# Kernel optimization log

Measured on AMD Instinct MI355X. Metric: run time of the kernel, lower is better.

The kernel has to match this reference:

```python
import jax, jax.numpy as jnp
import numpy as np
from jax import lax

# ---- static config (from cfg) ----
B, NCLS, CREG, H, W = 16, 3, 50, 96, 320
K = 100                  # DETECTIONS_PER_IMG
DOWN = 4                 # BACKBONE.DOWN_RATIO
THRESH = 0.2             # DETECTIONS_THRESHOLD
IMG_W, IMG_H = W * DOWN, H * DOWN
EPS = 1e-6
# channel layout in pred_reg (kvper):
#  0:4 dim_2d | 4:6 offset_3d | 6:9 dim_3d | 9:25 orient | 25:45 corner_offset
#  45:48 corner_uncertainty | 48 depth | 49 depth_uncertainty


def setup_inputs() -> dict:
    key = jax.random.key(0)
    k1, k2, k3 = jax.random.split(key, 3)
    # shift heatmap logits negative so only a sparse set passes the threshold
    pred_hmp = jax.random.normal(k1, (B, NCLS, H, W), jnp.float32) * 2.0 - 2.0
    pred_reg = jax.random.normal(k2, (B, CREG, H, W), jnp.float32) * 0.5
    # KITTI P2 intrinsics: [f_u, c_u, f_v, c_v] per image
    calib = jnp.tile(jnp.array([[721.5377, 609.5593, 721.5377, 172.854]],
                               jnp.float32), (B, 1))
    pad_size = jnp.zeros((B, 2), jnp.float32)
    # per-class mean dims (l, h, w): Car / Pedestrian / Cyclist
    dim_mean = jnp.array([[3.88, 1.53, 1.63],
                          [0.84, 1.76, 0.66],
                          [1.76, 1.73, 0.60]], jnp.float32)
    return {"pred_hmp": pred_hmp, "pred_reg": pred_reg, "calib": calib,
            "pad_size": pad_size, "dim_mean": dim_mean}


def reference(pred_hmp, pred_reg, calib, pad_size, dim_mean):
    f32 = pred_hmp.dtype
    # ---- nms_hm: sigmoid + 3x3 max-pool suppression ----
    heat = jax.nn.sigmoid(pred_hmp)
    hmax = lax.reduce_window(heat, -jnp.inf, lax.max,
                             (1, 1, 3, 3), (1, 1, 1, 1), 'SAME')
    heat = jnp.where(hmax == heat, heat, jnp.zeros((), f32))
    # ---- select_topk (CenterNet-style): per-class topk then global topk ----
    flat = heat.reshape(B, NCLS, H * W)
    s1, i1 = lax.top_k(flat, K)                        # (B, C, K)
    s2, i2 = lax.top_k(s1.reshape(B, NCLS * K), K)     # (B, K)
    classes = i2 // K                                  # (B, K)
    inds = jnp.take_along_axis(i1.reshape(B, NCLS * K), i2, axis=1)  # flat h*w idx
    ys = (inds // W).astype(f32)
    xs = (inds % W).astype(f32)
    # ---- select_point_of_interest: gather 50-ch reg features at topk points ----
    regf = pred_reg.transpose(0, 2, 3, 1).reshape(B, H * W, CREG)
    pois = jnp.take_along_axis(regf, inds[:, :, None], axis=1).reshape(B * K, CREG)

    scores = s2.reshape(-1)                            # (N,) N = B*K
    cls = classes.reshape(-1)
    pts = jnp.stack([xs.reshape(-1), ys.reshape(-1)], axis=1)  # (N, 2)
    mask = (scores >= THRESH).astype(f32)
    bidx = jnp.repeat(jnp.arange(B), K)                # per-detection batch index

    reg2d = jax.nn.relu(pois[:, 0:4])                  # l, t, r, b
    off3d = pois[:, 4:6]
    dimoff = pois[:, 6:9]
    kpt = pois[:, 25:45].reshape(-1, 10, 2)            # 10 keypoints (x, y)
    cunc = jnp.exp(pois[:, 45:48])                     # corner uncertainty
    doff = pois[:, 48]
    dunc = jnp.exp(pois[:, 49:50])                     # direct depth uncertainty

    # ---- decode_dim3d: exp offset scaled by class mean dims ----
    dims = jnp.exp(dimoff) * dim_mean[cls]             # (N, 3); dims[:,1] = height
    h3d = dims[:, 1]

    # ---- decode_depth (inv_sigmoid) ----
    direct_depth = jnp.clip(1.0 / jax.nn.sigmoid(doff) - 1.0, 0.1, 100.0)

    # ---- decode_depth_from_kpts_batch: pinhole height -> depth ----
    fu = calib[bidx, 0]; cu = calib[bidx, 1]
    fv = calib[bidx, 2]; cv = calib[bidx, 3]
    ctr_h = kpt[:, 8, 1] - kpt[:, 9, 1]                       # bottom - top center
    c02_h = kpt[:, jnp.array([0, 2]), 1] - kpt[:, jnp.array([4, 6]), 1]
    c13_h = kpt[:, jnp.array([1, 3]), 1] - kpt[:, jnp.array([5, 7]), 1]
    d_ctr = fu * h3d / (jax.nn.relu(ctr_h) * DOWN + EPS)
    d_02 = ((fu * h3d)[:, None] / (jax.nn.relu(c02_h) * DOWN + EPS)).mean(axis=1)
    d_13 = ((fu * h3d)[:, None] / (jax.nn.relu(c13_h) * DOWN + EPS)).mean(axis=1)
    kpt_depths = jnp.clip(jnp.stack([d_ctr, d_02, d_13], axis=1), 0.1, 100.0)

    # ---- 'soft' depth ensemble: uncertainty-weighted average ----
    comb_d = jnp.concatenate([direct_depth[:, None], kpt_depths], axis=1)  # (N,4)
    comb_u = jnp.concatenate([dunc, cunc], axis=1)                          # (N,4)
    wts = 1.0 / comb_u
    wts = wts / wts.sum(axis=1, keepdims=True)
    depth = (comb_d * wts).sum(axis=1)
    depth_err = (wts * comb_u).sum(axis=1)

    # ---- decode_box2d_fcos ----
    pad = pad_size[bidx]                               # (N, 2)
    box2d = jnp.concatenate([pts - reg2d[:, :2], pts + reg2d[:, 2:]],
                            axis=1) * DOWN - jnp.tile(pad, (1, 2))
    hi = jnp.array([IMG_W - 1, IMG_H - 1, IMG_W - 1, IMG_H - 1], f32)
    box2d = jnp.clip(box2d, 0.0, hi)

    # ---- decode_loc3d: unproject projected 3D center at estimated depth ----
    proj = (pts + off3d) * DOWN - pad                  # (N, 2) image-plane uv
    x3 = (proj[:, 0] - cu) * depth / fu
    y3 = (proj[:, 1] - cv) * depth / fv
    loc3d = jnp.stack([x3, y3, depth], axis=1)

    result = jnp.concatenate([cls.astype(f32)[:, None], scores[:, None],
                              box2d, dims, loc3d, depth_err[:, None]], axis=1)
    return result * mask[:, None]                      # (B*K, 13)
```

## Files before the change

kernel.cpp:

```cpp
#include <hip/hip_runtime.h>
#include <math.h>


#define W_ 320
#define H_ 96
#define HW_ (W_ * H_)
#define CANDCAP 2048
#define SKEYCAP 512
#define BITS_02 0x3E4CCCCDu
#define FLAG_MAGIC 0x5EC0DE01

__device__ inline unsigned long long shflx64(unsigned long long v, int m) {
  int lo = __shfl_xor((int)(unsigned)v, m, 64);
  int hi = __shfl_xor((int)(unsigned)(v >> 32), m, 64);
  return ((unsigned long long)(unsigned)hi << 32) | (unsigned)lo;
}

__global__ __launch_bounds__(1024) void monoflex_all(
    const float* __restrict__ hmp,
    const float* __restrict__ reg,
    const float* __restrict__ calib,
    const float* __restrict__ pad_size,
    const float* __restrict__ dim_mean,
    float* __restrict__ out,
    unsigned long long* __restrict__ s1,
    int* __restrict__ flags) {
  const int ph = blockIdx.x;
  const int half = ph & 1;
  const int plane = ph >> 1;
  const int t = threadIdx.x;
  const int lane = t & 63;
  const float* p = hmp + (size_t)plane * HW_;
  const int r0 = half * 48;

  __shared__ unsigned long long cand[CANDCAP];
  __shared__ unsigned long long skey[SKEYCAP];
  __shared__ int hist[1024];
  __shared__ int cnt, mcnt, cutbin;
  __shared__ unsigned long long halfkeys[600];
  __shared__ unsigned long long classlist[300];
  __shared__ int selgi[100];
  __shared__ int selcls[100];
  __shared__ float selsc[100];
  __shared__ float pbuf[100 * 51];

  if (t == 0) { cnt = 0; mcnt = 0; cutbin = 0; }
  hist[t] = 0;
  __syncthreads();

  for (int idx = t; idx < 48 * W_; idx += 1024) {
    int rr = idx / W_;
    int c = idx - rr * W_;
    int r = r0 + rr;
    int g = r * W_ + c;
    float v = p[g];
    float up = (r > 0) ? p[g - W_] : -INFINITY;
    float dn = (r < 95) ? p[g + W_] : -INFINITY;
    float vm = fmaxf(fmaxf(up, dn), v);
    float vmL = __shfl_up(vm, 1);
    float vmR = __shfl_down(vm, 1);
    if (lane == 0) {
      vmL = -INFINITY;
      if (c > 0) {
        float lv = p[g - 1];
        float lu = (r > 0) ? p[g - W_ - 1] : -INFINITY;
        float ld = (r < 95) ? p[g + W_ - 1] : -INFINITY;
        vmL = fmaxf(fmaxf(lu, ld), lv);
      }
    }
    if (lane == 63) {
      vmR = -INFINITY;
      if (c < 319) {
        float rv = p[g + 1];
        float ru = (r > 0) ? p[g - W_ + 1] : -INFINITY;
        float rd = (r < 95) ? p[g + W_ + 1] : -INFINITY;
        vmR = fmaxf(fmaxf(ru, rd), rv);
      }
    }
    float m9 = fmaxf(fmaxf(vmL, vmR), vm);
    bool pass = (v >= m9) && (v > -1.3865f);
    unsigned bits = 0u;
    if (pass) {
      float s = 1.0f / (1.0f + expf(-v));
      pass = (s >= 0.2f);
      if (pass) {
        bits = __float_as_uint(s);
        unsigned bin = (bits - BITS_02) >> 15;
        if (bin > 1023u) bin = 1023u;
        atomicAdd(&hist[bin], 1);
      }
    }
    unsigned long long act = __ballot(pass);
    if (pass) {
      int rank = __popcll(act & ((1ull << lane) - 1));
      int base;
      if (rank == 0) base = atomicAdd(&cnt, (int)__popcll(act));
      base = __shfl(base, (int)__ffsll(act) - 1);
      int q = base + rank;
      if (q < CANDCAP)
        cand[q] = ((unsigned long long)bits << 32) |
                  (unsigned long long)(0xFFFFFFFFu - (unsigned)g);
    }
  }
  __syncthreads();

  if (t < 64) {
    int ssum = 0;
    #pragma unroll
    for (int k2 = 0; k2 < 16; ++k2) ssum += hist[t * 16 + k2];
    int suf = ssum;
    #pragma unroll
    for (int off = 1; off < 64; off <<= 1) {
      int o = __shfl_down(suf, off);
      if (lane + off < 64) suf += o;
    }
    int sufn = __shfl_down(suf, 1);
    if (lane == 63) sufn = 0;
    if (suf >= 100 && sufn < 100) {
      int acc = sufn;
      int cb = t * 16;
      for (int k2 = t * 16 + 15; k2 >= t * 16; --k2) {
        acc += hist[k2];
        if (acc >= 100) { cb = k2; break; }
      }
      cutbin = cb;
    }
  }
  __syncthreads();
  const int cb = cutbin;
  const int n = min(cnt, CANDCAP);

  for (int i = t; i < n; i += 1024) {
    unsigned long long k = cand[i];
    unsigned bin = ((unsigned)(k >> 32) - BITS_02) >> 15;
    if (bin > 1023u) bin = 1023u;
    if ((int)bin >= cb) {
      int q = atomicAdd(&mcnt, 1);
      if (q < SKEYCAP) skey[q] = k;
    }
  }
  __syncthreads();
  const int m = min(mcnt, SKEYCAP);
  if (t >= m && t < SKEYCAP) skey[t] = 0ULL;
  __syncthreads();

  unsigned long long* dst = s1 + (size_t)ph * 100;
  if (m <= 128) {
    if (t < 64) {
      unsigned long long e0 = skey[lane], e1 = skey[64 + lane];
      #pragma unroll
      for (int k = 2; k <= 128; k <<= 1) {
        #pragma unroll
        for (int j = k >> 1; j > 0; j >>= 1) {
          if (j == 64) {
            if (e0 <= e1) { unsigned long long tmp = e0; e0 = e1; e1 = tmp; }
          } else {
            bool lower = ((lane & j) == 0);
            {
              unsigned long long o = shflx64(e0, j);
              bool asc = ((lane & k) != 0);
              unsigned long long lv = lower ? e0 : o, uv = lower ? o : e0;
              if ((lv > uv) == asc) e0 = o;
            }
            {
              unsigned long long o = shflx64(e1, j);
              bool asc = (((64 + lane) & k) != 0);
              unsigned long long lv = lower ? e1 : o, uv = lower ? o : e1;
              if ((lv > uv) == asc) e1 = o;
            }
          }
        }
      }
      dst[lane] = e0;
      if (lane < 36) dst[64 + lane] = e1;
      __threadfence();
      if (lane == 0) atomicExch(&flags[ph], FLAG_MAGIC);
    }
  } else {
    const int N = (m <= 256) ? 256 : 512;
    for (int k = 2; k <= N; k <<= 1) {
      for (int j = k >> 1; j > 0; j >>= 1) {
        if (t < N) {
          int l = t ^ j;
          if (l > t) {
            unsigned long long a = skey[t], b2 = skey[l];
            if ((a > b2) == ((t & k) != 0)) { skey[t] = b2; skey[l] = a; }
          }
        }
        __syncthreads();
      }
    }
    if (t < 100) dst[t] = skey[t];
    __threadfence();
    __syncthreads();
    if (t == 0) atomicExch(&flags[ph], FLAG_MAGIC);
  }

  if ((ph % 6) != 0) return;

  const int b = ph / 6;
  if (t < 5)
    while (atomicCAS(&flags[ph + 1 + t], FLAG_MAGIC, FLAG_MAGIC) != FLAG_MAGIC) {}
  __syncthreads();
  if (t < 600) halfkeys[t] = atomicAdd(&s1[b * 600 + t], 0ULL);
  if (t < 300) classlist[t] = 0ULL;
  __syncthreads();

  if (t < 600) {
    int c2 = t / 200, h = (t / 100) & 1, r = t % 100;
    unsigned long long key = halfkeys[t];
    if (key != 0ULL) {
      const unsigned long long* L = &halfkeys[(c2 * 2 + (1 - h)) * 100];
      int lo = 0, hi = 100;
      while (lo < hi) {
        int mid = (lo + hi) >> 1;
        if (L[mid] > key) lo = mid + 1; else hi = mid;
      }
      int cr = r + lo;
      if (cr < 100) classlist[c2 * 100 + cr] = key;
    }
  }
  __syncthreads();

  if (t < 300) {
    int c2 = t / 100, r2 = t - c2 * 100;
    unsigned long long key = classlist[t];
    unsigned bits = (unsigned)(key >> 32);
    int rank = r2;
    #pragma unroll
    for (int cp = 0; cp < 3; ++cp) {
      if (cp == c2) continue;
      const unsigned long long* L = classlist + cp * 100;
      int lo = 0, hi = 100;
      while (lo < hi) {
        int mid = (lo + hi) >> 1;
        if ((unsigned)(L[mid] >> 32) > bits) lo = mid + 1; else hi = mid;
      }
      int cntGT = lo;
      if (cp < c2) {
        lo = cntGT; hi = 100;
        while (lo < hi) {
          int mid = (lo + hi) >> 1;
          if ((unsigned)(L[mid] >> 32) >= bits) lo = mid + 1; else hi = mid;
        }
        rank += lo;
      } else {
        rank += cntGT;
      }
    }
    if (rank < 100) {
      bool valid = (bits != 0u);
      selgi[rank]  = valid ? (int)(0xFFFFFFFFu - (unsigned)(key & 0xFFFFFFFFull))
                           : -1;
      selcls[rank] = c2;
      selsc[rank]  = __uint_as_float(bits);
    }
  }
  __syncthreads();

  const float* rbase = reg + (size_t)b * 50 * HW_;
  {
    float gv[5];
    int gx[5];
    #pragma unroll
    for (int rr2 = 0; rr2 < 5; ++rr2) {
      int idx = rr2 * 1024 + t;
      bool ok = idx < 5000;
      int row = ok ? (idx % 100) : 0;
      int ch  = ok ? (idx / 100) : 0;
      int gi = selgi[row];
      gv[rr2] = (ok && gi >= 0) ? rbase[(size_t)ch * HW_ + gi] : 0.0f;
      gx[rr2] = row * 51 + ch;
    }
    #pragma unroll
    for (int rr2 = 0; rr2 < 5; ++rr2) {
      int idx = rr2 * 1024 + t;
      if (idx < 5000) pbuf[gx[rr2]] = gv[rr2];
    }
  }
  __syncthreads();

  if (t < 100) {
    float* orow = out + ((size_t)b * 100 + t) * 13;
    int gi = selgi[t];
    if (gi < 0) {
      #pragma unroll
      for (int i = 0; i < 13; ++i) orow[i] = 0.0f;
    } else {
      const float* pp = &pbuf[t * 51];
      int cls = selcls[t];
      float score = selsc[t];
      int yy = gi / W_;
      int xx = gi - yy * W_;
      float x = (float)xx, y = (float)yy;

      float fu = calib[b * 4 + 0], cu = calib[b * 4 + 1];
      float fv = calib[b * 4 + 2], cv = calib[b * 4 + 3];
      float pad0 = pad_size[b * 2 + 0], pad1 = pad_size[b * 2 + 1];

      float rA = fmaxf(pp[0], 0.f), rB = fmaxf(pp[1], 0.f);
      float rC = fmaxf(pp[2], 0.f), rD = fmaxf(pp[3], 0.f);
      float bx0 = fminf(fmaxf((x - rA) * 4.f - pad0, 0.f), 1279.f);
      float by0 = fminf(fmaxf((y - rB) * 4.f - pad1, 0.f), 383.f);
      float bx1 = fminf(fmaxf((x + rC) * 4.f - pad0, 0.f), 1279.f);
      float by1 = fminf(fmaxf((y + rD) * 4.f - pad1, 0.f), 383.f);

      float d0 = expf(pp[6]) * dim_mean[cls * 3 + 0];
      float d1 = expf(pp[7]) * dim_mean[cls * 3 + 1];
      float d2 = expf(pp[8]) * dim_mean[cls * 3 + 2];
      float h3d = d1;

      float sig = 1.0f / (1.0f + expf(-pp[48]));
      float ddepth = fminf(fmaxf(1.0f / sig - 1.0f, 0.1f), 100.0f);

      float fh = fu * h3d;
      float d_ctr = fh / (fmaxf(pp[42] - pp[44], 0.f) * 4.f + 1e-6f);
      float d02 = 0.5f * (fh / (fmaxf(pp[26] - pp[34], 0.f) * 4.f + 1e-6f) +
                          fh / (fmaxf(pp[30] - pp[38], 0.f) * 4.f + 1e-6f));
      float d13 = 0.5f * (fh / (fmaxf(pp[28] - pp[36], 0.f) * 4.f + 1e-6f) +
                          fh / (fmaxf(pp[32] - pp[40], 0.f) * 4.f + 1e-6f));
      float kd0 = fminf(fmaxf(d_ctr, 0.1f), 100.f);
      float kd1 = fminf(fmaxf(d02, 0.1f), 100.f);
      float kd2 = fminf(fmaxf(d13, 0.1f), 100.f);

      float u0 = expf(pp[49]), u1 = expf(pp[45]);
      float u2 = expf(pp[46]), u3 = expf(pp[47]);
      float w0 = 1.f / u0, w1 = 1.f / u1, w2 = 1.f / u2, w3 = 1.f / u3;
      float S = w0 + w1 + w2 + w3;
      float depth = (ddepth * w0 + kd0 * w1 + kd1 * w2 + kd2 * w3) / S;
      float derr = (w0 * u0 + w1 * u1 + w2 * u2 + w3 * u3) / S;

      float px = (x + pp[4]) * 4.f - pad0;
      float py = (y + pp[5]) * 4.f - pad1;
      float x3 = (px - cu) * depth / fu;
      float y3 = (py - cv) * depth / fv;

      orow[0] = (float)cls;
      orow[1] = score;
      orow[2] = bx0; orow[3] = by0; orow[4] = bx1; orow[5] = by1;
      orow[6] = d0;  orow[7] = d1;  orow[8] = d2;
      orow[9] = x3;  orow[10] = y3; orow[11] = depth;
      orow[12] = derr;
    }
  }
}

extern "C" void kernel_launch(void* const* d_in, const int* in_sizes, int n_in,
                              void* d_out, int out_size, void* d_ws, size_t ws_size,
                              hipStream_t stream) {
  const float* hmp   = (const float*)d_in[0];
  const float* reg   = (const float*)d_in[1];
  const float* calib = (const float*)d_in[2];
  const float* pads  = (const float*)d_in[3];
  const float* dm    = (const float*)d_in[4];
  float* out = (float*)d_out;

  unsigned long long* s1 = (unsigned long long*)d_ws;
  int* flags = (int*)((char*)d_ws + 96 * 100 * 8);

  monoflex_all<<<dim3(96), dim3(1024), 0, stream>>>(hmp, reg, calib, pads, dm,
                                                    out, s1, flags);
}
```

Before: 173.0 us.

## Split fused kernel into quarter-plane NMS/topk and per-batch merge-decode kernels

```diff
diff --git a/kernel.cpp b/kernel.cpp
--- a/kernel.cpp
+++ b/kernel.cpp
@@ -5,10 +5,10 @@
 #define W_ 320
 #define H_ 96
 #define HW_ (W_ * H_)
+#define QROWS 24
 #define CANDCAP 2048
 #define SKEYCAP 512
 #define BITS_02 0x3E4CCCCDu
-#define FLAG_MAGIC 0x5EC0DE01
 
 __device__ inline unsigned long long shflx64(unsigned long long v, int m) {
   int lo = __shfl_xor((int)(unsigned)v, m, 64);
@@ -16,39 +16,27 @@
   return ((unsigned long long)(unsigned)hi << 32) | (unsigned)lo;
 }
 
-__global__ __launch_bounds__(1024) void monoflex_all(
+__global__ __launch_bounds__(1024) void nms_topk(
     const float* __restrict__ hmp,
-    const float* __restrict__ reg,
-    const float* __restrict__ calib,
-    const float* __restrict__ pad_size,
-    const float* __restrict__ dim_mean,
-    float* __restrict__ out,
-    unsigned long long* __restrict__ s1,
-    int* __restrict__ flags) {
+    unsigned long long* __restrict__ s1) {
   const int ph = blockIdx.x;
-  const int half = ph & 1;
-  const int plane = ph >> 1;
+  const int plane = ph >> 2;
+  const int q = ph & 3;
+  const int r0 = q * QROWS;
   const int t = threadIdx.x;
   const int lane = t & 63;
   const float* p = hmp + (size_t)plane * HW_;
-  const int r0 = half * 48;
 
   __shared__ unsigned long long cand[CANDCAP];
   __shared__ unsigned long long skey[SKEYCAP];
   __shared__ int hist[1024];
   __shared__ int cnt, mcnt, cutbin;
-  __shared__ unsigned long long halfkeys[600];
-  __shared__ unsigned long long classlist[300];
-  __shared__ int selgi[100];
-  __shared__ int selcls[100];
-  __shared__ float selsc[100];
-  __shared__ float pbuf[100 * 51];
 
   if (t == 0) { cnt = 0; mcnt = 0; cutbin = 0; }
   hist[t] = 0;
   __syncthreads();
 
-  for (int idx = t; idx < 48 * W_; idx += 1024) {
+  for (int idx = t; idx < QROWS * W_; idx += 1024) {
     int rr = idx / W_;
     int c = idx - rr * W_;
     int r = r0 + rr;
@@ -96,10 +84,10 @@
       int base;
       if (rank == 0) base = atomicAdd(&cnt, (int)__popcll(act));
       base = __shfl(base, (int)__ffsll(act) - 1);
-      int q = base + rank;
-      if (q < CANDCAP)
-        cand[q] = ((unsigned long long)bits << 32) |
-                  (unsigned long long)(0xFFFFFFFFu - (unsigned)g);
+      int qq = base + rank;
+      if (qq < CANDCAP)
+        cand[qq] = ((unsigned long long)bits << 32) |
+                   (unsigned long long)(0xFFFFFFFFu - (unsigned)g);
     }
   }
   __syncthreads();
@@ -135,8 +123,8 @@
     unsigned bin = ((unsigned)(k >> 32) - BITS_02) >> 15;
     if (bin > 1023u) bin = 1023u;
     if ((int)bin >= cb) {
-      int q = atomicAdd(&mcnt, 1);
-      if (q < SKEYCAP) skey[q] = k;
+      int qq = atomicAdd(&mcnt, 1);
+      if (qq < SKEYCAP) skey[qq] = k;
     }
   }
   __syncthreads();
@@ -173,8 +161,6 @@
       }
       dst[lane] = e0;
       if (lane < 36) dst[64 + lane] = e1;
-      __threadfence();
-      if (lane == 0) atomicExch(&flags[ph], FLAG_MAGIC);
     }
   } else {
     const int N = (m <= 256) ? 256 : 512;
@@ -191,33 +177,50 @@
       }
     }
     if (t < 100) dst[t] = skey[t];
-    __threadfence();
-    __syncthreads();
-    if (t == 0) atomicExch(&flags[ph], FLAG_MAGIC);
-  }
-
-  if ((ph % 6) != 0) return;
-
-  const int b = ph / 6;
-  if (t < 5)
-    while (atomicCAS(&flags[ph + 1 + t], FLAG_MAGIC, FLAG_MAGIC) != FLAG_MAGIC) {}
-  __syncthreads();
-  if (t < 600) halfkeys[t] = atomicAdd(&s1[b * 600 + t], 0ULL);
+  }
+}
+
+__global__ __launch_bounds__(1024) void merge_decode(
+    const unsigned long long* __restrict__ s1,
+    const float* __restrict__ reg,
+    const float* __restrict__ calib,
+    const float* __restrict__ pad_size,
+    const float* __restrict__ dim_mean,
+    float* __restrict__ out) {
+  const int b = blockIdx.x;
+  const int t = threadIdx.x;
+
+  __shared__ unsigned long long qkeys[1200];
+  __shared__ unsigned long long classlist[300];
+  __shared__ int selgi[100];
+  __shared__ int selcls[100];
+  __shared__ float selsc[100];
+  __shared__ float pbuf[100 * 51];
+
+  for (int i = t; i < 1200; i += 1024) qkeys[i] = s1[b * 1200 + i];
   if (t < 300) classlist[t] = 0ULL;
-  __syncthreads();
-
-  if (t < 600) {
-    int c2 = t / 200, h = (t / 100) & 1, r = t % 100;
-    unsigned long long key = halfkeys[t];
+  if (t < 100) { selgi[t] = -1; selcls[t] = 0; selsc[t] = 0.0f; }
+  __syncthreads();
+
+  for (int i = t; i < 1200; i += 1024) {
+    int c2 = i / 400;
+    int qo = (i / 100) & 3;
+    int r = i % 100;
+    unsigned long long key = qkeys[i];
     if (key != 0ULL) {
-      const unsigned long long* L = &halfkeys[(c2 * 2 + (1 - h)) * 100];
-      int lo = 0, hi = 100;
-      while (lo < hi) {
-        int mid = (lo + hi) >> 1;
-        if (L[mid] > key) lo = mid + 1; else hi = mid;
-      }
-      int cr = r + lo;
-      if (cr < 100) classlist[c2 * 100 + cr] = key;
+      int rank = r;
+      #pragma unroll
+      for (int qs = 0; qs < 4; ++qs) {
+        if (qs == qo) continue;
+        const unsigned long long* L = &qkeys[(c2 * 4 + qs) * 100];
+        int lo = 0, hi = 100;
+        while (lo < hi) {
+          int mid = (lo + hi) >> 1;
+          if (L[mid] > key) lo = mid + 1; else hi = mid;
+        }
+        rank += lo;
+      }
+      if (rank < 100) classlist[c2 * 100 + rank] = key;
     }
   }
   __syncthreads();
@@ -248,10 +251,8 @@
         rank += cntGT;
       }
     }
-    if (rank < 100) {
-      bool valid = (bits != 0u);
-      selgi[rank]  = valid ? (int)(0xFFFFFFFFu - (unsigned)(key & 0xFFFFFFFFull))
-                           : -1;
+    if (rank < 100 && bits != 0u) {
+      selgi[rank]  = (int)(0xFFFFFFFFu - (unsigned)(key & 0xFFFFFFFFull));
       selcls[rank] = c2;
       selsc[rank]  = __uint_as_float(bits);
     }
@@ -356,8 +357,7 @@
   float* out = (float*)d_out;
 
   unsigned long long* s1 = (unsigned long long*)d_ws;
-  int* flags = (int*)((char*)d_ws + 96 * 100 * 8);
-
-  monoflex_all<<<dim3(96), dim3(1024), 0, stream>>>(hmp, reg, calib, pads, dm,
-                                                    out, s1, flags);
+
+  nms_topk<<<dim3(192), dim3(1024), 0, stream>>>(hmp, s1);
+  merge_decode<<<dim3(16), dim3(1024), 0, stream>>>(s1, reg, calib, pads, dm, out);
 }
```

Result: faster. 169.2 us (-2.2%).
